# Kernel optimization log

Measured on AMD Instinct MI355X. Metric: run time of the kernel, lower is better.

## Reference

```python
import jax, jax.numpy as jnp
import numpy as np

B, D, L = 16, 64, 2048
NUM_TOKENS = 8192


def setup_inputs() -> dict:
    key = jax.random.key(0)
    k1, k2 = jax.random.split(key)
    z_e = jax.random.normal(k1, (B, D, L), dtype=jnp.float32)
    codebook = jax.random.normal(k2, (NUM_TOKENS, D), dtype=jnp.float32)
    return {"z_e": z_e, "codebook": codebook}


def reference(z_e, codebook):
    # z_e: [B, D, L] -> per-position vectors [B, L, D]
    x = jnp.transpose(z_e, (0, 2, 1))          # [B, L, D]
    xf = x.reshape(-1, x.shape[-1])            # [N, D], N = B*L
    x2 = jnp.sum(xf * xf, axis=-1, keepdims=True)            # [N, 1]
    c2 = jnp.sum(codebook * codebook, axis=-1)               # [K]
    d2 = x2 - 2.0 * (xf @ codebook.T) + c2[None, :]          # [N, K]
    idx = jnp.argmin(d2, axis=-1)                            # [N]
    zq = codebook[idx]                                        # [N, D] gather
    zq = zq.reshape(x.shape)                                  # [B, L, D]
    # straight-through with codebook stop-gradient (code_sg=True)
    zq_st = x + jax.lax.stop_gradient(zq - x)                 # [B, L, D]
    v_q = jnp.transpose(zq_st, (0, 2, 1))                     # [B, D, L]
    indices = idx.reshape(z_e.shape[0], -1)                   # [B, L]
    return v_q, indices
```

## Files before the change

### kernel.cpp

```cpp
#include <hip/hip_runtime.h>
#include <hip/hip_bf16.h>
#include <hip/hip_fp16.h>
#include <cstdint>

#define BB 16
#define DD 64
#define LL 2048
#define NQ (BB*LL)
#define KK 8192
#define VQ_SIZE (BB*DD*LL)
#define CHUNK 256
#define NCH (KK/CHUNK)
#define NG 64
#define QSL 256
#define QPS (NQ/QSL)
#define MARGIN 0.80f

typedef __attribute__((ext_vector_type(8))) short short8;
typedef __attribute__((ext_vector_type(4))) float f32x4;
typedef unsigned long long u64;


static __device__ inline short f2bf(float f) {
    __hip_bfloat16 h = __float2bfloat16(f);
    return __builtin_bit_cast(short, h);
}

#define FMIN_DPP(v, ctrl)                                                     \
    do {                                                                      \
        int _vi = __float_as_int(v);                                          \
        int _sh = __builtin_amdgcn_update_dpp(_vi, _vi, (ctrl), 0xf, 0xf, false); \
        (v) = fminf((v), __int_as_float(_sh));                                \
    } while (0)

#define FMAX_DPP(v, ctrl)                                                     \
    do {                                                                      \
        int _vi = __float_as_int(v);                                          \
        int _sh = __builtin_amdgcn_update_dpp(_vi, _vi, (ctrl), 0xf, 0xf, false); \
        (v) = fmaxf((v), __int_as_float(_sh));                                \
    } while (0)

__global__ __launch_bounds__(256) void prep_x(const float* __restrict__ ze,
                                              short* __restrict__ xb) {
    __shared__ float t[64][65];
    const int b = blockIdx.x;
    const int l0 = blockIdx.y * 64;
    const int tid = threadIdx.x;
    #pragma unroll
    for (int it = 0; it < 4; ++it) {
        int id = it * 256 + tid;
        int d = id >> 4;
        int lw = (id & 15) * 4;
        const float4 v = *(const float4*)(ze + ((size_t)b * DD + d) * LL + l0 + lw);
        t[d][lw + 0] = v.x; t[d][lw + 1] = v.y; t[d][lw + 2] = v.z; t[d][lw + 3] = v.w;
    }
    __syncthreads();
    #pragma unroll
    for (int it = 0; it < 2; ++it) {
        int id = it * 256 + tid;
        int lr = id >> 3;
        int u = id & 7;
        short8 o;
        #pragma unroll
        for (int e = 0; e < 8; ++e) o[e] = f2bf(t[u * 8 + e][lr]);
        *(short8*)(xb + (size_t)(b * LL + l0 + lr) * DD + u * 8) = o;
    }
}

__global__ __launch_bounds__(256) void prep_xf(const float* __restrict__ ze,
                                               float* __restrict__ xf) {
    __shared__ float t[64][65];
    const int b = blockIdx.x;
    const int l0 = blockIdx.y * 64;
    const int tid = threadIdx.x;
    #pragma unroll
    for (int it = 0; it < 4; ++it) {
        int id = it * 256 + tid;
        int d = id >> 4;
        int lw = (id & 15) * 4;
        const float4 v = *(const float4*)(ze + ((size_t)b * DD + d) * LL + l0 + lw);
        t[d][lw + 0] = v.x; t[d][lw + 1] = v.y; t[d][lw + 2] = v.z; t[d][lw + 3] = v.w;
    }
    __syncthreads();
    #pragma unroll
    for (int it = 0; it < 4; ++it) {
        int id = it * 256 + tid;
        int row = id >> 4;
        int u = id & 15;
        float4 o = make_float4(t[4 * u + 0][row], t[4 * u + 1][row],
                               t[4 * u + 2][row], t[4 * u + 3][row]);
        *(float4*)(xf + (size_t)(b * LL + l0 + row) * DD + u * 4) = o;
    }
}

__global__ __launch_bounds__(256) void prep_nh2(const float* __restrict__ cbf,
                                                float* __restrict__ nh2) {
    int k = blockIdx.x * 256 + threadIdx.x;
    const float4* c4 = (const float4*)(cbf + (size_t)k * DD);
    float s = 0.f;
    #pragma unroll
    for (int i = 0; i < DD / 4; ++i) {
        float4 v = c4[i];
        s += v.x * v.x + v.y * v.y + v.z * v.z + v.w * v.w;
    }
    nh2[k] = -0.5f * s;
}

__global__ __launch_bounds__(256) void vq_screen(const float* __restrict__ cbf,
                                                 const float* __restrict__ nh2,
                                                 const short* __restrict__ xb,
                                                 __half* __restrict__ cmaxG) {
    __shared__ short cbt[CHUNK * 64];
    __shared__ float sh2[CHUNK];
    const int tid = threadIdx.x;
    const int lane = tid & 63;
    const int wid = tid >> 6;
    const int kbase = blockIdx.y * CHUNK;
    const int qbase = blockIdx.x * 256 + wid * 64;
    const int r16 = lane & 15, g = lane >> 4;

    #pragma unroll
    for (int it = 0; it < 8; ++it) {
        int id = it * 256 + tid;
        int row = id >> 3;
        int u = id & 7;
        const float4 lo = *(const float4*)(cbf + (size_t)(kbase + row) * 64 + u * 8);
        const float4 hi = *(const float4*)(cbf + (size_t)(kbase + row) * 64 + u * 8 + 4);
        short8 o;
        o[0] = f2bf(lo.x); o[1] = f2bf(lo.y); o[2] = f2bf(lo.z); o[3] = f2bf(lo.w);
        o[4] = f2bf(hi.x); o[5] = f2bf(hi.y); o[6] = f2bf(hi.z); o[7] = f2bf(hi.w);
        *(short8*)(&cbt[row * 64 + ((u ^ (row & 7)) * 8)]) = o;
    }
    sh2[tid] = nh2[kbase + tid];
    __syncthreads();

    short8 a[4][2];
    #pragma unroll
    for (int t = 0; t < 4; ++t)
        #pragma unroll
        for (int ks = 0; ks < 2; ++ks)
            a[t][ks] = *(const short8*)(xb + (size_t)(qbase + t * 16 + r16) * 64 + ks * 32 + g * 8);

    float rm[2][4][4];
    #pragma unroll
    for (int h = 0; h < 2; ++h)
        #pragma unroll
        for (int t = 0; t < 4; ++t)
            #pragma unroll
            for (int j = 0; j < 4; ++j) rm[h][t][j] = -3.4e38f;

    #pragma unroll
    for (int cs = 0; cs < CHUNK / 16; ++cs) {
        const int rowb = cs * 16 + r16;
        const float nh = sh2[rowb];
        const f32x4 ci = {nh, nh, nh, nh};
        const short8 b0 = *(const short8*)(&cbt[rowb * 64 + ((g ^ (rowb & 7)) * 8)]);
        const short8 b1 = *(const short8*)(&cbt[rowb * 64 + (((g + 4) ^ (rowb & 7)) * 8)]);
        #pragma unroll
        for (int t = 0; t < 4; ++t) {
            f32x4 acc = __builtin_amdgcn_mfma_f32_16x16x32_bf16(a[t][0], b0, ci, 0, 0, 0);
            acc = __builtin_amdgcn_mfma_f32_16x16x32_bf16(a[t][1], b1, acc, 0, 0, 0);
            rm[cs >> 3][t][0] = fmaxf(rm[cs >> 3][t][0], acc[0]);
            rm[cs >> 3][t][1] = fmaxf(rm[cs >> 3][t][1], acc[1]);
            rm[cs >> 3][t][2] = fmaxf(rm[cs >> 3][t][2], acc[2]);
            rm[cs >> 3][t][3] = fmaxf(rm[cs >> 3][t][3], acc[3]);
        }
    }

    #pragma unroll
    for (int h = 0; h < 2; ++h)
        #pragma unroll
        for (int t = 0; t < 4; ++t)
            #pragma unroll
            for (int j = 0; j < 4; ++j) {
                FMAX_DPP(rm[h][t][j], 0x111);
                FMAX_DPP(rm[h][t][j], 0x112);
                FMAX_DPP(rm[h][t][j], 0x114);
                FMAX_DPP(rm[h][t][j], 0x118);
            }

    if (r16 == 15) {
        #pragma unroll
        for (int h = 0; h < 2; ++h)
            #pragma unroll
            for (int t = 0; t < 4; ++t)
                #pragma unroll
                for (int j = 0; j < 4; ++j)
                    cmaxG[(size_t)(blockIdx.y * 2 + h) * NQ + (qbase + t * 16 + g * 4 + j)] =
                        __float2half_rd(rm[h][t][j]);
    }
}

template <bool FINE>
__global__ __launch_bounds__(256) void vq_cand(const __half* __restrict__ cmaxG,
                                               u64* __restrict__ mask64,
                                               uint32_t* __restrict__ mask32,
                                               u64* __restrict__ keys) {
    const int q = blockIdx.x * 256 + threadIdx.x;
    float m = -3.4e38f;
    #pragma unroll
    for (int j = 0; j < NG; ++j)
        m = fmaxf(m, __half2float(cmaxG[(size_t)j * NQ + q]));
    keys[q] = ~0ULL;
    const float thr = m - MARGIN;
    if (FINE) {
        u64 mm = 0;
        #pragma unroll
        for (int j = 0; j < NG; ++j)
            if (__half2float(cmaxG[(size_t)j * NQ + q]) >= thr) mm |= (1ULL << j);
        mask64[q] = mm;
    } else {
        uint32_t mm = 0;
        #pragma unroll
        for (int j = 0; j < NCH; ++j) {
            bool a0 = __half2float(cmaxG[(size_t)(2 * j) * NQ + q]) >= thr;
            bool a1 = __half2float(cmaxG[(size_t)(2 * j + 1) * NQ + q]) >= thr;
            if (a0 || a1) mm |= (1u << j);
        }
        mask32[q] = mm;
    }
}

template <bool FINE>
__global__ __launch_bounds__(256, 2) void vq_exact(const float* __restrict__ xf,
                                                   const float* __restrict__ cbf,
                                                   const float* __restrict__ nh2,
                                                   const u64* __restrict__ mask64,
                                                   const uint32_t* __restrict__ mask32,
                                                   u64* __restrict__ keys) {
    const int ch = blockIdx.x;
    const int slice = blockIdx.y;
    const int lane = threadIdx.x & 63;
    const int wid = threadIdx.x >> 6;
    const int kb = ch * CHUNK + wid * 64;
    const int k = kb + lane;
    const int qs = slice * QPS;

    u64 b0, b1;
    if (FINE) {
        const int grp = ch * 2 + (wid >> 1);
        u64 m0 = mask64[qs + lane];
        u64 m1 = mask64[qs + 64 + lane];
        b0 = __ballot(((m0 >> grp) & 1ULL) != 0);
        b1 = __ballot(((m1 >> grp) & 1ULL) != 0);
    } else {
        uint32_t m0 = mask32[qs + lane];
        uint32_t m1 = mask32[qs + 64 + lane];
        b0 = __ballot(((m0 >> ch) & 1u) != 0);
        b1 = __ballot(((m1 >> ch) & 1u) != 0);
    }
    u64 words[2];
    {
        uint32_t lo = __builtin_amdgcn_readfirstlane((uint32_t)b0);
        uint32_t hi = __builtin_amdgcn_readfirstlane((uint32_t)(b0 >> 32));
        words[0] = ((u64)hi << 32) | lo;
        lo = __builtin_amdgcn_readfirstlane((uint32_t)b1);
        hi = __builtin_amdgcn_readfirstlane((uint32_t)(b1 >> 32));
        words[1] = ((u64)hi << 32) | lo;
    }
    if (!(words[0] | words[1])) return;

    f32x4 cdv[16];
    const f32x4* cb4 = (const f32x4*)(cbf + (size_t)k * DD);
    #pragma unroll
    for (int i = 0; i < 16; ++i) cdv[i] = cb4[i];
    const float nh2k = nh2[k];

    #pragma unroll 1
    for (int w = 0; w < 2; ++w) {
        u64 sw = words[w];
        while (sw) {
            const int bit = __ffsll((long long)sw) - 1;
            sw &= sw - 1;
            const int q = qs + w * 64 + bit;
            const f32x4* xr4 = (const f32x4*)(xf + (size_t)q * DD);
            f32x4 xv[16];
            #pragma unroll
            for (int i = 0; i < 16; ++i) xv[i] = xr4[i];

            float a0 = 0.f, a1 = 0.f, a2 = 0.f, a3 = 0.f;
            #pragma unroll
            for (int i = 0; i < 16; ++i) {
                a0 = fmaf(xv[i].x, cdv[i].x, a0);
                a1 = fmaf(xv[i].y, cdv[i].y, a1);
                a2 = fmaf(xv[i].z, cdv[i].z, a2);
                a3 = fmaf(xv[i].w, cdv[i].w, a3);
            }
            float val = -(((a0 + a1) + (a2 + a3)) + nh2k);

            float mn = val;
            FMIN_DPP(mn, 0x111);
            FMIN_DPP(mn, 0x112);
            FMIN_DPP(mn, 0x114);
            FMIN_DPP(mn, 0x118);
            FMIN_DPP(mn, 0x142);
            FMIN_DPP(mn, 0x143);
            const float mnall = __uint_as_float(
                __builtin_amdgcn_readlane(__float_as_uint(mn), 63));

            u64 mk = __ballot(val == mnall);
            int srcl = __ffsll((long long)mk) - 1;
            uint32_t uu = __float_as_uint(mnall);
            uint32_t ub = ((int)uu < 0) ? ~uu : (uu | 0x80000000u);
            u64 key = ((u64)ub << 32) | (unsigned)(kb + srcl);
            if (lane == 0) atomicMin(&keys[q], key);
        }
    }
}

__global__ __launch_bounds__(256) void vq_gather(const float* __restrict__ cb,
                                                 const u64* __restrict__ keys,
                                                 float* __restrict__ vq,
                                                 float* __restrict__ oidx) {
    int t = blockIdx.x * 256 + threadIdx.x;
    int l = t & (LL - 1);
    int bd = t >> 11;
    int d = bd & 63;
    int b = bd >> 6;
    int idx = (int)(unsigned)(keys[b * LL + l] & 0x1FFFu);
    vq[t] = cb[idx * DD + d];
    if (d == 0) oidx[b * LL + l] = (float)idx;
}

extern "C" void kernel_launch(void* const* d_in, const int* in_sizes, int n_in,
                              void* d_out, int out_size, void* d_ws, size_t ws_size,
                              hipStream_t stream) {
    const float* ze = (const float*)d_in[0];
    const float* cb = (const float*)d_in[1];
    float* out = (float*)d_out;

    short* xb = (short*)d_out;
    __half* cmaxG = (__half*)((char*)d_out + (size_t)NQ * DD * 2);
    float* xf = (float*)d_out;
    float* nh2 = (float*)d_ws;
    u64* keys = (u64*)((char*)d_ws + (size_t)KK * 4);
    u64* mask64 = (u64*)((char*)d_ws + (size_t)288 * 1024);
    uint32_t* mask32 = (uint32_t*)(out + VQ_SIZE);
    float* oidx = out + VQ_SIZE;

    const bool fine = ws_size >= (size_t)(544 * 1024);

    dim3 gx(BB, LL / 64);
    prep_x<<<gx, 256, 0, stream>>>(ze, xb);
    prep_nh2<<<KK / 256, 256, 0, stream>>>(cb, nh2);

    dim3 gs(NQ / 256, NCH);
    vq_screen<<<gs, 256, 0, stream>>>(cb, nh2, xb, cmaxG);

    if (fine) vq_cand<true><<<NQ / 256, 256, 0, stream>>>(cmaxG, mask64, mask32, keys);
    else      vq_cand<false><<<NQ / 256, 256, 0, stream>>>(cmaxG, mask64, mask32, keys);

    prep_xf<<<gx, 256, 0, stream>>>(ze, xf);

    dim3 ge(NCH, QSL);
    if (fine) vq_exact<true><<<ge, 256, 0, stream>>>(xf, cb, nh2, mask64, mask32, keys);
    else      vq_exact<false><<<ge, 256, 0, stream>>>(xf, cb, nh2, mask64, mask32, keys);

    vq_gather<<<VQ_SIZE / 256, 256, 0, stream>>>(cb, keys, out, oidx);
}
```

Before: 158.7 us.

## Precompute swizzled bf16 codebook and double queries per wave in screen kernel

Adds a prep kernel that converts the codebook to bf16 once, already in the XOR-swizzled layout, so each screen block only copies shorts into LDS instead of reloading and converting fp32 per block. The screen kernel also processes 128 queries per wave (512 per block), halving the grid and reusing each staged codebook chunk across twice as many MFMAs. The accumulator loop is restructured to do one half-chunk at a time to limit register growth from the larger query tile. This raises register pressure and lowers the block count, and the new path runs only when the workspace is large enough.

Measured after the change: 161.1 us. Within noise of the previous version (+1.5%).

```diff
diff --git a/kernel.cpp b/kernel.cpp
--- a/kernel.cpp
+++ b/kernel.cpp
@@ -67,6 +67,20 @@
     }
 }
 
+__global__ __launch_bounds__(256) void prep_cb16(const float* __restrict__ cbf,
+                                                 short* __restrict__ cb16s) {
+    int gi = blockIdx.x * 256 + threadIdx.x;
+    int row = gi >> 3;
+    int w = gi & 7;
+    int col = (w ^ (row & 7)) * 8;
+    const float4 lo = *(const float4*)(cbf + (size_t)row * DD + col);
+    const float4 hi = *(const float4*)(cbf + (size_t)row * DD + col + 4);
+    short8 o;
+    o[0] = f2bf(lo.x); o[1] = f2bf(lo.y); o[2] = f2bf(lo.z); o[3] = f2bf(lo.w);
+    o[4] = f2bf(hi.x); o[5] = f2bf(hi.y); o[6] = f2bf(hi.z); o[7] = f2bf(hi.w);
+    *(short8*)(cb16s + (size_t)gi * 8) = o;
+}
+
 __global__ __launch_bounds__(256) void prep_xf(const float* __restrict__ ze,
                                                float* __restrict__ xf) {
     __shared__ float t[64][65];
@@ -106,7 +120,9 @@
     nh2[k] = -0.5f * s;
 }
 
+template <bool CB16>
 __global__ __launch_bounds__(256) void vq_screen(const float* __restrict__ cbf,
+                                                 const short* __restrict__ cb16s,
                                                  const float* __restrict__ nh2,
                                                  const short* __restrict__ xb,
                                                  __half* __restrict__ cmaxG) {
@@ -116,78 +132,84 @@
     const int lane = tid & 63;
     const int wid = tid >> 6;
     const int kbase = blockIdx.y * CHUNK;
-    const int qbase = blockIdx.x * 256 + wid * 64;
+    const int qbase = blockIdx.x * 512 + wid * 128;
     const int r16 = lane & 15, g = lane >> 4;
 
-    #pragma unroll
-    for (int it = 0; it < 8; ++it) {
-        int id = it * 256 + tid;
-        int row = id >> 3;
-        int u = id & 7;
-        const float4 lo = *(const float4*)(cbf + (size_t)(kbase + row) * 64 + u * 8);
-        const float4 hi = *(const float4*)(cbf + (size_t)(kbase + row) * 64 + u * 8 + 4);
-        short8 o;
-        o[0] = f2bf(lo.x); o[1] = f2bf(lo.y); o[2] = f2bf(lo.z); o[3] = f2bf(lo.w);
-        o[4] = f2bf(hi.x); o[5] = f2bf(hi.y); o[6] = f2bf(hi.z); o[7] = f2bf(hi.w);
-        *(short8*)(&cbt[row * 64 + ((u ^ (row & 7)) * 8)]) = o;
+    if (CB16) {
+        #pragma unroll
+        for (int it = 0; it < 8; ++it) {
+            int id = it * 256 + tid;
+            *(short8*)(&cbt[id * 8]) =
+                *(const short8*)(cb16s + (size_t)kbase * 64 + (size_t)id * 8);
+        }
+    } else {
+        #pragma unroll
+        for (int it = 0; it < 8; ++it) {
+            int id = it * 256 + tid;
+            int row = id >> 3;
+            int u = id & 7;
+            const float4 lo = *(const float4*)(cbf + (size_t)(kbase + row) * 64 + u * 8);
+            const float4 hi = *(const float4*)(cbf + (size_t)(kbase + row) * 64 + u * 8 + 4);
+            short8 o;
+            o[0] = f2bf(lo.x); o[1] = f2bf(lo.y); o[2] = f2bf(lo.z); o[3] = f2bf(lo.w);
+            o[4] = f2bf(hi.x); o[5] = f2bf(hi.y); o[6] = f2bf(hi.z); o[7] = f2bf(hi.w);
+            *(short8*)(&cbt[row * 64 + ((u ^ (row & 7)) * 8)]) = o;
+        }
     }
     sh2[tid] = nh2[kbase + tid];
     __syncthreads();
 
-    short8 a[4][2];
-    #pragma unroll
-    for (int t = 0; t < 4; ++t)
+    short8 a[8][2];
+    #pragma unroll
+    for (int t = 0; t < 8; ++t)
         #pragma unroll
         for (int ks = 0; ks < 2; ++ks)
             a[t][ks] = *(const short8*)(xb + (size_t)(qbase + t * 16 + r16) * 64 + ks * 32 + g * 8);
 
-    float rm[2][4][4];
-    #pragma unroll
-    for (int h = 0; h < 2; ++h)
-        #pragma unroll
-        for (int t = 0; t < 4; ++t)
-            #pragma unroll
-            for (int j = 0; j < 4; ++j) rm[h][t][j] = -3.4e38f;
-
-    #pragma unroll
-    for (int cs = 0; cs < CHUNK / 16; ++cs) {
-        const int rowb = cs * 16 + r16;
-        const float nh = sh2[rowb];
-        const f32x4 ci = {nh, nh, nh, nh};
-        const short8 b0 = *(const short8*)(&cbt[rowb * 64 + ((g ^ (rowb & 7)) * 8)]);
-        const short8 b1 = *(const short8*)(&cbt[rowb * 64 + (((g + 4) ^ (rowb & 7)) * 8)]);
-        #pragma unroll
-        for (int t = 0; t < 4; ++t) {
-            f32x4 acc = __builtin_amdgcn_mfma_f32_16x16x32_bf16(a[t][0], b0, ci, 0, 0, 0);
-            acc = __builtin_amdgcn_mfma_f32_16x16x32_bf16(a[t][1], b1, acc, 0, 0, 0);
-            rm[cs >> 3][t][0] = fmaxf(rm[cs >> 3][t][0], acc[0]);
-            rm[cs >> 3][t][1] = fmaxf(rm[cs >> 3][t][1], acc[1]);
-            rm[cs >> 3][t][2] = fmaxf(rm[cs >> 3][t][2], acc[2]);
-            rm[cs >> 3][t][3] = fmaxf(rm[cs >> 3][t][3], acc[3]);
-        }
-    }
-
-    #pragma unroll
-    for (int h = 0; h < 2; ++h)
-        #pragma unroll
-        for (int t = 0; t < 4; ++t)
+    float rm[8][4];
+    #pragma unroll
+    for (int h = 0; h < 2; ++h) {
+        #pragma unroll
+        for (int t = 0; t < 8; ++t)
+            #pragma unroll
+            for (int j = 0; j < 4; ++j) rm[t][j] = -3.4e38f;
+
+        #pragma unroll
+        for (int cs = h * 8; cs < h * 8 + 8; ++cs) {
+            const int rowb = cs * 16 + r16;
+            const float nh = sh2[rowb];
+            const f32x4 ci = {nh, nh, nh, nh};
+            const short8 b0 = *(const short8*)(&cbt[rowb * 64 + ((g ^ (rowb & 7)) * 8)]);
+            const short8 b1 = *(const short8*)(&cbt[rowb * 64 + (((g + 4) ^ (rowb & 7)) * 8)]);
+            #pragma unroll
+            for (int t = 0; t < 8; ++t) {
+                f32x4 acc = __builtin_amdgcn_mfma_f32_16x16x32_bf16(a[t][0], b0, ci, 0, 0, 0);
+                acc = __builtin_amdgcn_mfma_f32_16x16x32_bf16(a[t][1], b1, acc, 0, 0, 0);
+                rm[t][0] = fmaxf(rm[t][0], acc[0]);
+                rm[t][1] = fmaxf(rm[t][1], acc[1]);
+                rm[t][2] = fmaxf(rm[t][2], acc[2]);
+                rm[t][3] = fmaxf(rm[t][3], acc[3]);
+            }
+        }
+
+        #pragma unroll
+        for (int t = 0; t < 8; ++t)
             #pragma unroll
             for (int j = 0; j < 4; ++j) {
-                FMAX_DPP(rm[h][t][j], 0x111);
-                FMAX_DPP(rm[h][t][j], 0x112);
-                FMAX_DPP(rm[h][t][j], 0x114);
-                FMAX_DPP(rm[h][t][j], 0x118);
+                FMAX_DPP(rm[t][j], 0x111);
+                FMAX_DPP(rm[t][j], 0x112);
+                FMAX_DPP(rm[t][j], 0x114);
+                FMAX_DPP(rm[t][j], 0x118);
             }
 
-    if (r16 == 15) {
-        #pragma unroll
-        for (int h = 0; h < 2; ++h)
-            #pragma unroll
-            for (int t = 0; t < 4; ++t)
+        if (r16 == 15) {
+            #pragma unroll
+            for (int t = 0; t < 8; ++t)
                 #pragma unroll
                 for (int j = 0; j < 4; ++j)
                     cmaxG[(size_t)(blockIdx.y * 2 + h) * NQ + (qbase + t * 16 + g * 4 + j)] =
-                        __float2half_rd(rm[h][t][j]);
+                        __float2half_rd(rm[t][j]);
+        }
     }
 }
 
@@ -335,17 +357,21 @@
     float* nh2 = (float*)d_ws;
     u64* keys = (u64*)((char*)d_ws + (size_t)KK * 4);
     u64* mask64 = (u64*)((char*)d_ws + (size_t)288 * 1024);
+    short* cb16s = (short*)((char*)d_ws + (size_t)544 * 1024);
     uint32_t* mask32 = (uint32_t*)(out + VQ_SIZE);
     float* oidx = out + VQ_SIZE;
 
     const bool fine = ws_size >= (size_t)(544 * 1024);
+    const bool cb16 = ws_size >= (size_t)(544 * 1024 + KK * DD * 2);
 
     dim3 gx(BB, LL / 64);
     prep_x<<<gx, 256, 0, stream>>>(ze, xb);
     prep_nh2<<<KK / 256, 256, 0, stream>>>(cb, nh2);
-
-    dim3 gs(NQ / 256, NCH);
-    vq_screen<<<gs, 256, 0, stream>>>(cb, nh2, xb, cmaxG);
+    if (cb16) prep_cb16<<<(KK * 8) / 256, 256, 0, stream>>>(cb, cb16s);
+
+    dim3 gs(NQ / 512, NCH);
+    if (cb16) vq_screen<true><<<gs, 256, 0, stream>>>(cb, cb16s, nh2, xb, cmaxG);
+    else      vq_screen<false><<<gs, 256, 0, stream>>>(cb, cb16s, nh2, xb, cmaxG);
 
     if (fine) vq_cand<true><<<NQ / 256, 256, 0, stream>>>(cmaxG, mask64, mask32, keys);
     else      vq_cand<false><<<NQ / 256, 256, 0, stream>>>(cmaxG, mask64, mask32, keys);
```
